# Optimization experiments

Hardware: AMD Instinct MI355X
Metric: run time of the kernel (lower is better)

The kernel has to match this reference:

```python
import jax, jax.numpy as jnp
import numpy as np
from jax import lax

EPS = 1e-8

def setup_inputs() -> dict:
    key = jax.random.key(0)
    k1, k2, k3, k4 = jax.random.split(key, 4)
    b, ic, oc, ks, sd, h, w = 16, 512, 512, 3, 512, 64, 64
    x = jax.random.normal(k1, (b, ic, h, w), dtype=jnp.float32)
    style = jax.random.normal(k2, (b, sd), dtype=jnp.float32)
    # kaiming_normal_(fan_in, linear): std = 1/sqrt(ic*ks*ks)
    weight = jax.random.normal(k3, (oc, ic, ks, ks), dtype=jnp.float32) / np.sqrt(ic * ks * ks)
    bias = jnp.zeros((oc,), dtype=jnp.float32)
    # nn.Linear default init ~ U(-1/sqrt(sd), 1/sqrt(sd)); normal approx is fine for a baseline
    mod_w = jax.random.normal(k4, (ic, sd), dtype=jnp.float32) / np.sqrt(sd)
    mod_b = jnp.ones((ic,), dtype=jnp.float32)  # bias initialized to 1.0 in the module
    return {"x": x, "style": style, "weight": weight, "bias": bias, "mod_w": mod_w, "mod_b": mod_b}

def reference(x, style, weight, bias, mod_w, mod_b):
    b, ic, h, w = x.shape
    oc, _, ks, _ = weight.shape
    # style modulation: [b, ic]
    s = style @ mod_w.T + mod_b
    # per-sample modulated weights: [b, oc, ic, k, k]
    wmod = weight[None] * s[:, None, :, None, None]
    # demodulation
    demod = lax.rsqrt(jnp.sum(wmod * wmod, axis=(2, 3, 4)) + EPS)  # [b, oc]
    wmod = wmod * demod[:, :, None, None, None]
    pad = ks // 2
    # grouped conv with groups=b == per-sample conv: vmap over batch
    def conv1(xi, wi):  # xi: [ic,h,w], wi: [oc,ic,k,k]
        return lax.conv_general_dilated(
            xi[None], wi, window_strides=(1, 1),
            padding=[(pad, pad), (pad, pad)],
            dimension_numbers=("NCHW", "OIHW", "NCHW"))[0]
    out = jax.vmap(conv1)(x, wmod)  # [b, oc, h, w]
    return out + bias[None, :, None, None]
```

## Files before the change

kernel.cpp:

```cpp
#include <hip/hip_runtime.h>
#include <hip/hip_bf16.h>


typedef __bf16 bf16x8 __attribute__((ext_vector_type(8)));
typedef float  f32x4  __attribute__((ext_vector_type(4)));

#define IC   512
#define OC   512
#define HW   4096
#define KTOT 4608

typedef __attribute__((address_space(3))) unsigned lds_u32;
typedef const __attribute__((address_space(1))) unsigned glb_u32;
#define GLL16(gsrc, ldst) \
    __builtin_amdgcn_global_load_lds((glb_u32*)(gsrc), (lds_u32*)(ldst), 16, 0, 0)
#define VMW(N) asm volatile("s_waitcnt vmcnt(" #N ")" ::: "memory")
#define BAR()  asm volatile("s_barrier" ::: "memory")

__global__ __launch_bounds__(256) void style_mod_kernel(
    const float* __restrict__ style, const float* __restrict__ mod_w,
    const float* __restrict__ mod_b, float* __restrict__ s_out)
{
    int pair = blockIdx.x * 4 + (threadIdx.x >> 6);
    int lane = threadIdx.x & 63;
    int b = pair >> 9;
    int i = pair & 511;
    const float4* sv = (const float4*)(style + b * 512);
    const float4* wv = (const float4*)(mod_w + i * 512);
    float4 a0 = sv[lane * 2], a1 = sv[lane * 2 + 1];
    float4 w0 = wv[lane * 2], w1 = wv[lane * 2 + 1];
    float sum = a0.x*w0.x + a0.y*w0.y + a0.z*w0.z + a0.w*w0.w
              + a1.x*w1.x + a1.y*w1.y + a1.z*w1.z + a1.w*w1.w;
    #pragma unroll
    for (int off = 32; off; off >>= 1) sum += __shfl_xor(sum, off);
    if (lane == 0) s_out[pair] = sum + mod_b[i];
}

__global__ __launch_bounds__(256) void wmod_kernel(
    const float* __restrict__ weight,
    const float* __restrict__ s_in,
    __hip_bfloat16* __restrict__ wmod)
{
    int b  = blockIdx.x >> 9;
    int oc = blockIdx.x & 511;
    __shared__ float s_sh[512];
    __shared__ float red[256];
    int t = threadIdx.x;
    s_sh[t]       = s_in[b * 512 + t];
    s_sh[t + 256] = s_in[b * 512 + t + 256];
    __syncthreads();
    const float* wrow = weight + (size_t)oc * KTOT;
    float partial = 0.f;
    for (int e = t; e < KTOT; e += 256) {
        float v = wrow[e] * s_sh[e / 9];
        partial += v * v;
    }
    red[t] = partial;
    __syncthreads();
    #pragma unroll
    for (int off = 128; off; off >>= 1) {
        if (t < off) red[t] += red[t + off];
        __syncthreads();
    }
    float demod = rsqrtf(red[0] + 1e-8f);
    __hip_bfloat16* dst = wmod + (size_t)blockIdx.x * KTOT;
    for (int ep = t; ep < KTOT; ep += 256) {
        int tap = ep >> 9, ic = ep & 511;
        dst[ep] = __float2bfloat16(wrow[ic * 9 + tap] * s_sh[ic] * demod);
    }
}

__global__ void zero_row_kernel(__hip_bfloat16* xT) {
    ((unsigned*)(xT + ((size_t)blockIdx.x * 4097 + 4096) * 512))[threadIdx.x] = 0u;
}

__global__ __launch_bounds__(256) void xpose_kernel(
    const float* __restrict__ x, __hip_bfloat16* __restrict__ xT)
{
    __shared__ __align__(16) float tile[64][68];
    int b = blockIdx.z, ic0 = blockIdx.y * 64, p0 = blockIdx.x * 64;
    int t = threadIdx.x;
    const float* xb = x + ((size_t)b * 512 + ic0) * 4096 + p0;
    int rr = t >> 4, cc = (t & 15) * 4;
    #pragma unroll
    for (int i = 0; i < 4; ++i) {
        float4 v = *(const float4*)(xb + (size_t)(rr + i * 16) * 4096 + cc);
        *(float4*)&tile[rr + i * 16][cc] = v;
    }
    __syncthreads();
    int pr = t >> 2, io = (t & 3) * 16;
    __hip_bfloat16 obuf[16];
    #pragma unroll
    for (int j = 0; j < 16; ++j) obuf[j] = __float2bfloat16(tile[io + j][pr]);
    __hip_bfloat16* dst = xT + ((size_t)b * 4097 + p0 + pr) * 512 + ic0 + io;
    *(uint4*)dst       = *(uint4*)&obuf[0];
    *(uint4*)(dst + 8) = *(uint4*)&obuf[8];
}

__global__ __launch_bounds__(512, 2) void conv_kernel(
    const __hip_bfloat16* __restrict__ xT,
    const __hip_bfloat16* __restrict__ wmod,
    const float* __restrict__ bias,
    float* __restrict__ out)
{
    __shared__ __align__(16) __hip_bfloat16 Ash[4][256 * 32];
    __shared__ __align__(16) __hip_bfloat16 Bsh[4][256 * 32];

    const int t    = threadIdx.x;
    const int lane = t & 63;
    const int wid  = t >> 6;
    const int wm   = wid >> 2;
    const int wn   = wid & 3;
    const int lr   = lane & 15;
    const int lq   = lane >> 4;

    int bid = blockIdx.x;
    int xcd = bid & 7, idx = bid >> 3;
    int oc1 = idx & 1;
    int nt  = (idx >> 1) & 15;
    int bb  = (idx >> 5) & 1;
    int b   = xcd * 2 + bb;
    int oc0 = oc1 * 256, n0 = nt * 256;

    const __hip_bfloat16* wb = wmod + (size_t)(b * 512 + oc0) * KTOT;
    const __hip_bfloat16* xb = xT + (size_t)b * 4097 * 512;

    const int qoff = (((t & 3) ^ ((t >> 3) & 3)) * 8);
    const int srow = t >> 2;
    const int p0g  = n0 + srow;
    const int y0p  = p0g >> 6, x0p = p0g & 63;

    const __hip_bfloat16* pA0 = wb + (size_t)srow * KTOT + qoff;
    const __hip_bfloat16* pA1 = pA0 + (size_t)128 * KTOT;

    const int swq = (lq ^ ((lr >> 1) & 3)) * 8;
    const int arb = (wm * 128 + lr) * 32 + swq;
    const int brb = (wn * 64  + lr) * 32 + swq;

    f32x4 acc[8][4] = {};

    auto bptrs = [&](int tap, const __hip_bfloat16*& P0, const __hip_bfloat16*& P1) {
        int dy = tap / 3 - 1, dx = tap % 3 - 1;
        int sy = y0p + dy, sx = x0p + dx;
        int pix0 = ((((unsigned)sy)  < 64u) & (((unsigned)sx) < 64u)) ? ((sy  << 6) + sx) : 4096;
        int sy1 = sy + 2;
        int pix1 = ((((unsigned)sy1) < 64u) & (((unsigned)sx) < 64u)) ? ((sy1 << 6) + sx) : 4096;
        P0 = xb + (size_t)pix0 * 512 + qoff;
        P1 = xb + (size_t)pix1 * 512 + qoff;
    };

#define STAGE(SB, PA_OFF, Q0, Q1, B_OFF) { \
    GLL16(pA0 + (PA_OFF), &Ash[SB][t * 8]); \
    GLL16(pA1 + (PA_OFF), &Ash[SB][(t + 512) * 8]); \
    GLL16((Q0) + (B_OFF), &Bsh[SB][t * 8]); \
    GLL16((Q1) + (B_OFF), &Bsh[SB][(t + 512) * 8]); }

#define COMPUTE(CB) { \
    bf16x8 af[8], bf[4]; \
    _Pragma("unroll") for (int mi = 0; mi < 8; ++mi) \
        af[mi] = *(const bf16x8*)(&Ash[CB][arb + mi * 512]); \
    _Pragma("unroll") for (int ni = 0; ni < 4; ++ni) \
        bf[ni] = *(const bf16x8*)(&Bsh[CB][brb + ni * 512]); \
    __builtin_amdgcn_s_setprio(1); \
    _Pragma("unroll") for (int mi = 0; mi < 8; ++mi) \
        _Pragma("unroll") for (int ni = 0; ni < 4; ++ni) \
            acc[mi][ni] = __builtin_amdgcn_mfma_f32_16x16x32_bf16( \
                af[mi], bf[ni], acc[mi][ni], 0, 0, 0); \
    __builtin_amdgcn_s_setprio(0); }

    const __hip_bfloat16 *pB0, *pB1, *nB0, *nB1;
    bptrs(0, pB0, pB1);

    STAGE(0, 0,  pB0, pB1, 0);
    STAGE(1, 32, pB0, pB1, 32);
    STAGE(2, 64, pB0, pB1, 64);
    VMW(8);
    BAR();

    for (int tap = 0; tap < 8; ++tap) {
        bptrs(tap + 1, nB0, nB1);
        #pragma unroll
        for (int ch = 0; ch < 16; ++ch) {
            if (ch < 13) { STAGE((ch + 3) & 3, (ch + 3) * 32, pB0, pB1, (ch + 3) * 32); }
            else         { STAGE((ch + 3) & 3, (ch + 3) * 32, nB0, nB1, (ch - 13) * 32); }
            COMPUTE(ch & 3);
            VMW(8);
            BAR();
        }
        pA0 += 512; pA1 += 512;
        pB0 = nB0; pB1 = nB1;
    }
    #pragma unroll
    for (int ch = 0; ch < 16; ++ch) {
        if (ch <= 12) { STAGE((ch + 3) & 3, (ch + 3) * 32, pB0, pB1, (ch + 3) * 32); }
        COMPUTE(ch & 3);
        if      (ch < 13)  { VMW(8); BAR(); }
        else if (ch == 13) { VMW(4); BAR(); }
        else if (ch == 14) { VMW(0); BAR(); }
    }
#undef STAGE
#undef COMPUTE

    #pragma unroll
    for (int mi = 0; mi < 8; ++mi) {
        int oc = oc0 + wm * 128 + mi * 16 + lq * 4;
        #pragma unroll
        for (int ni = 0; ni < 4; ++ni) {
            int n = n0 + wn * 64 + ni * 16 + lr;
            #pragma unroll
            for (int v = 0; v < 4; ++v) {
                float r = acc[mi][ni][v] + bias[oc + v];
                out[((size_t)(b * OC + oc + v)) * HW + n] = r;
            }
        }
    }
}

extern "C" void kernel_launch(void* const* d_in, const int* in_sizes, int n_in,
                              void* d_out, int out_size, void* d_ws, size_t ws_size,
                              hipStream_t stream) {
    const float* x      = (const float*)d_in[0];
    const float* style  = (const float*)d_in[1];
    const float* weight = (const float*)d_in[2];
    const float* bias   = (const float*)d_in[3];
    const float* mod_w  = (const float*)d_in[4];
    const float* mod_b  = (const float*)d_in[5];
    float* out = (float*)d_out;

    float* s_ws = (float*)d_ws;
    __hip_bfloat16* wmod = (__hip_bfloat16*)((char*)d_ws + 32768);
    __hip_bfloat16* xT   = (__hip_bfloat16*)((char*)d_ws + 32768 + (size_t)16 * 512 * KTOT * 2);

    style_mod_kernel<<<2048, 256, 0, stream>>>(style, mod_w, mod_b, s_ws);
    wmod_kernel<<<16 * 512, 256, 0, stream>>>(weight, s_ws, wmod);
    zero_row_kernel<<<16, 256, 0, stream>>>(xT);
    dim3 tgrid(64, 8, 16);
    xpose_kernel<<<tgrid, 256, 0, stream>>>(x, xT);
    conv_kernel<<<512, 512, 0, stream>>>(xT, wmod, bias, out);
}
```

Measured before the change: 379.4 us.

## Restructure conv mainloop into 64-wide double buffer and batch wmod per oc

The conv kernel moves from a 4-stage 32-wide K pipeline to a 2-buffer 64-wide K pipeline with a new XOR swizzle. Each 64-K step is split into eight quarter phases that interleave LDS fragment loads, global-to-LDS loads and MFMA groups, separated by barriers and explicit lgkm/vm waits. The wmod kernel now handles one output channel for all 16 samples, loading the weight row once and computing demod from per-ic squared sums times s squared, which avoids re-reading weights per sample. The cost is many more barriers per step and larger LDS use in wmod, which may lower occupancy.

```diff
diff --git a/kernel.cpp b/kernel.cpp
--- a/kernel.cpp
+++ b/kernel.cpp
@@ -14,8 +14,12 @@
 typedef const __attribute__((address_space(1))) unsigned glb_u32;
 #define GLL16(gsrc, ldst) \
     __builtin_amdgcn_global_load_lds((glb_u32*)(gsrc), (lds_u32*)(ldst), 16, 0, 0)
-#define VMW(N) asm volatile("s_waitcnt vmcnt(" #N ")" ::: "memory")
-#define BAR()  asm volatile("s_barrier" ::: "memory")
+#define BAR()   asm volatile("s_barrier" ::: "memory")
+#define LGKM0() asm volatile("s_waitcnt lgkmcnt(0)" ::: "memory")
+
+template<int N> __device__ __forceinline__ void vmw() {
+    asm volatile("s_waitcnt vmcnt(%0)" :: "n"(N) : "memory");
+}
 
 __global__ __launch_bounds__(256) void style_mod_kernel(
     const float* __restrict__ style, const float* __restrict__ mod_w,
@@ -41,32 +45,41 @@
     const float* __restrict__ s_in,
     __hip_bfloat16* __restrict__ wmod)
 {
-    int b  = blockIdx.x >> 9;
-    int oc = blockIdx.x & 511;
-    __shared__ float s_sh[512];
-    __shared__ float red[256];
+    int oc = blockIdx.x;
+    __shared__ float w_sh[4608];
+    __shared__ float s_sh[8192];
+    __shared__ float q_sh[512];
+    __shared__ float demod_sh[16];
     int t = threadIdx.x;
-    s_sh[t]       = s_in[b * 512 + t];
-    s_sh[t + 256] = s_in[b * 512 + t + 256];
+    const float* wrow = weight + (size_t)oc * KTOT;
+    for (int e = t; e < 4608; e += 256) w_sh[e] = wrow[e];
+    for (int e = t; e < 8192; e += 256) s_sh[e] = s_in[e];
     __syncthreads();
-    const float* wrow = weight + (size_t)oc * KTOT;
-    float partial = 0.f;
-    for (int e = t; e < KTOT; e += 256) {
-        float v = wrow[e] * s_sh[e / 9];
-        partial += v * v;
-    }
-    red[t] = partial;
+    for (int ic = t; ic < 512; ic += 256) {
+        float q = 0.f;
+        #pragma unroll
+        for (int tap = 0; tap < 9; ++tap) { float w = w_sh[ic * 9 + tap]; q += w * w; }
+        q_sh[ic] = q;
+    }
     __syncthreads();
-    #pragma unroll
-    for (int off = 128; off; off >>= 1) {
-        if (t < off) red[t] += red[t + off];
-        __syncthreads();
-    }
-    float demod = rsqrtf(red[0] + 1e-8f);
-    __hip_bfloat16* dst = wmod + (size_t)blockIdx.x * KTOT;
-    for (int ep = t; ep < KTOT; ep += 256) {
-        int tap = ep >> 9, ic = ep & 511;
-        dst[ep] = __float2bfloat16(wrow[ic * 9 + tap] * s_sh[ic] * demod);
+    int bb = t >> 4, li = t & 15;
+    float part = 0.f;
+    for (int ic = li; ic < 512; ic += 16) {
+        float sv = s_sh[bb * 512 + ic];
+        part += q_sh[ic] * sv * sv;
+    }
+    #pragma unroll
+    for (int off = 8; off; off >>= 1) part += __shfl_xor(part, off, 16);
+    if (li == 0) demod_sh[bb] = rsqrtf(part + 1e-8f);
+    __syncthreads();
+    for (int b2 = 0; b2 < 16; ++b2) {
+        float dm = demod_sh[b2];
+        const float* srow = s_sh + b2 * 512;
+        __hip_bfloat16* dst = wmod + ((size_t)b2 * 512 + oc) * KTOT;
+        for (int ep = t; ep < 4608; ep += 256) {
+            int tap = ep >> 9, ic = ep & 511;
+            dst[ep] = __float2bfloat16(w_sh[ic * 9 + tap] * srow[ic] * dm);
+        }
     }
 }
 
@@ -103,8 +116,12 @@
     const float* __restrict__ bias,
     float* __restrict__ out)
 {
-    __shared__ __align__(16) __hip_bfloat16 Ash[4][256 * 32];
-    __shared__ __align__(16) __hip_bfloat16 Bsh[4][256 * 32];
+    __shared__ __align__(16) __hip_bfloat16 Ash[2][256 * 64];
+    __shared__ __align__(16) __hip_bfloat16 Bsh[2][256 * 64];
+    __hip_bfloat16* const Ash0 = &Ash[0][0];
+    __hip_bfloat16* const Ash1 = &Ash[1][0];
+    __hip_bfloat16* const Bsh0 = &Bsh[0][0];
+    __hip_bfloat16* const Bsh1 = &Bsh[1][0];
 
     const int t    = threadIdx.x;
     const int lane = t & 63;
@@ -125,81 +142,127 @@
     const __hip_bfloat16* wb = wmod + (size_t)(b * 512 + oc0) * KTOT;
     const __hip_bfloat16* xb = xT + (size_t)b * 4097 * 512;
 
-    const int qoff = (((t & 3) ^ ((t >> 3) & 3)) * 8);
-    const int srow = t >> 2;
+    const int qoff = (((t & 7) ^ ((t >> 3) & 7)) * 8);
+    const int srow = t >> 3;
     const int p0g  = n0 + srow;
     const int y0p  = p0g >> 6, x0p = p0g & 63;
 
     const __hip_bfloat16* pA0 = wb + (size_t)srow * KTOT + qoff;
-    const __hip_bfloat16* pA1 = pA0 + (size_t)128 * KTOT;
-
-    const int swq = (lq ^ ((lr >> 1) & 3)) * 8;
-    const int arb = (wm * 128 + lr) * 32 + swq;
-    const int brb = (wn * 64  + lr) * 32 + swq;
+    const __hip_bfloat16* pA1 = pA0 + (size_t)64  * KTOT;
+    const __hip_bfloat16* pA2 = pA0 + (size_t)128 * KTOT;
+    const __hip_bfloat16* pA3 = pA0 + (size_t)192 * KTOT;
+
+    const int aoff0 = (wm * 128 + lr) * 64 + ((lq       ^ (lr & 7)) * 8);
+    const int aoff1 = (wm * 128 + lr) * 64 + (((4 + lq) ^ (lr & 7)) * 8);
+    const int boff0 = (wn * 64  + lr) * 64 + ((lq       ^ (lr & 7)) * 8);
+    const int boff1 = (wn * 64  + lr) * 64 + (((4 + lq) ^ (lr & 7)) * 8);
 
     f32x4 acc[8][4] = {};
-
-    auto bptrs = [&](int tap, const __hip_bfloat16*& P0, const __hip_bfloat16*& P1) {
+    bf16x8 a0[8], a1[8], b0[4], b1[4];
+
+    const __hip_bfloat16 *pB0_, *pB1_, *pB2_, *pB3_, *nB0, *nB1, *nB2, *nB3;
+    auto bptrs = [&](int tap, const __hip_bfloat16*& P0, const __hip_bfloat16*& P1,
+                     const __hip_bfloat16*& P2, const __hip_bfloat16*& P3) {
         int dy = tap / 3 - 1, dx = tap % 3 - 1;
-        int sy = y0p + dy, sx = x0p + dx;
-        int pix0 = ((((unsigned)sy)  < 64u) & (((unsigned)sx) < 64u)) ? ((sy  << 6) + sx) : 4096;
-        int sy1 = sy + 2;
-        int pix1 = ((((unsigned)sy1) < 64u) & (((unsigned)sx) < 64u)) ? ((sy1 << 6) + sx) : 4096;
-        P0 = xb + (size_t)pix0 * 512 + qoff;
-        P1 = xb + (size_t)pix1 * 512 + qoff;
+        int sx = x0p + dx;
+        bool okx = ((unsigned)sx < 64u);
+        int sy0 = y0p + dy;
+        int q0 = (okx & ((unsigned)(sy0    ) < 64u)) ? ((sy0    ) * 64 + sx) : 4096;
+        int q1 = (okx & ((unsigned)(sy0 + 1) < 64u)) ? ((sy0 + 1) * 64 + sx) : 4096;
+        int q2 = (okx & ((unsigned)(sy0 + 2) < 64u)) ? ((sy0 + 2) * 64 + sx) : 4096;
+        int q3 = (okx & ((unsigned)(sy0 + 3) < 64u)) ? ((sy0 + 3) * 64 + sx) : 4096;
+        P0 = xb + (size_t)q0 * 512 + qoff;
+        P1 = xb + (size_t)q1 * 512 + qoff;
+        P2 = xb + (size_t)q2 * 512 + qoff;
+        P3 = xb + (size_t)q3 * 512 + qoff;
     };
 
-#define STAGE(SB, PA_OFF, Q0, Q1, B_OFF) { \
-    GLL16(pA0 + (PA_OFF), &Ash[SB][t * 8]); \
-    GLL16(pA1 + (PA_OFF), &Ash[SB][(t + 512) * 8]); \
-    GLL16((Q0) + (B_OFF), &Bsh[SB][t * 8]); \
-    GLL16((Q1) + (B_OFF), &Bsh[SB][(t + 512) * 8]); }
-
-#define COMPUTE(CB) { \
-    bf16x8 af[8], bf[4]; \
-    _Pragma("unroll") for (int mi = 0; mi < 8; ++mi) \
-        af[mi] = *(const bf16x8*)(&Ash[CB][arb + mi * 512]); \
-    _Pragma("unroll") for (int ni = 0; ni < 4; ++ni) \
-        bf[ni] = *(const bf16x8*)(&Bsh[CB][brb + ni * 512]); \
+#define MF16(M0, AF, BF) { \
     __builtin_amdgcn_s_setprio(1); \
-    _Pragma("unroll") for (int mi = 0; mi < 8; ++mi) \
+    _Pragma("unroll") for (int mi = 0; mi < 4; ++mi) \
         _Pragma("unroll") for (int ni = 0; ni < 4; ++ni) \
-            acc[mi][ni] = __builtin_amdgcn_mfma_f32_16x16x32_bf16( \
-                af[mi], bf[ni], acc[mi][ni], 0, 0, 0); \
+            acc[(M0) + mi][ni] = __builtin_amdgcn_mfma_f32_16x16x32_bf16( \
+                AF[(M0) + mi], BF[ni], acc[(M0) + mi][ni], 0, 0, 0); \
     __builtin_amdgcn_s_setprio(0); }
 
-    const __hip_bfloat16 *pB0, *pB1, *nB0, *nB1;
-    bptrs(0, pB0, pB1);
-
-    STAGE(0, 0,  pB0, pB1, 0);
-    STAGE(1, 32, pB0, pB1, 32);
-    STAGE(2, 64, pB0, pB1, 64);
-    VMW(8);
+#define ITER_BODY(CT1, SCA, SCB, SP0, SP1, SP2, SP3, TAIL, VN4) { \
+     \
+    _Pragma("unroll") for (int mi = 0; mi < 8; ++mi) a0[mi] = *(const bf16x8*)&Ash0[aoff0 + mi * 1024]; \
+    _Pragma("unroll") for (int ni = 0; ni < 4; ++ni) b0[ni] = *(const bf16x8*)&Bsh0[boff0 + ni * 1024]; \
+    GLL16(pB0_ + (CT1), &Bsh1[t * 8]); GLL16(pB1_ + (CT1), &Bsh1[(t + 512) * 8]); \
+    BAR(); LGKM0(); \
+    MF16(0, a0, b0); \
+    BAR(); \
+     \
+    _Pragma("unroll") for (int mi = 0; mi < 8; ++mi) a1[mi] = *(const bf16x8*)&Ash0[aoff1 + mi * 1024]; \
+    GLL16(pB2_ + (CT1), &Bsh1[(t + 1024) * 8]); GLL16(pB3_ + (CT1), &Bsh1[(t + 1536) * 8]); \
+    BAR(); LGKM0(); \
+    MF16(4, a0, b0); \
+    BAR(); \
+     \
+    _Pragma("unroll") for (int ni = 0; ni < 4; ++ni) b1[ni] = *(const bf16x8*)&Bsh0[boff1 + ni * 1024]; \
+    if (!(TAIL)) { GLL16(pA0 + (SCA), &Ash0[t * 8]); GLL16(pA1 + (SCA), &Ash0[(t + 512) * 8]); } \
+    BAR(); LGKM0(); \
+    MF16(0, a1, b1); \
+    BAR(); \
+     \
+    if (!(TAIL)) { GLL16(pA2 + (SCA), &Ash0[(t + 1024) * 8]); GLL16(pA3 + (SCA), &Ash0[(t + 1536) * 8]); } \
+    BAR(); \
+    MF16(4, a1, b1); \
+    vmw<VN4>(); \
+    BAR(); \
+     \
+    _Pragma("unroll") for (int mi = 0; mi < 8; ++mi) a0[mi] = *(const bf16x8*)&Ash1[aoff0 + mi * 1024]; \
+    _Pragma("unroll") for (int ni = 0; ni < 4; ++ni) b0[ni] = *(const bf16x8*)&Bsh1[boff0 + ni * 1024]; \
+    if (!(TAIL)) { GLL16((SP0) + (SCB), &Bsh0[t * 8]); GLL16((SP1) + (SCB), &Bsh0[(t + 512) * 8]); } \
+    BAR(); LGKM0(); \
+    MF16(0, a0, b0); \
+    BAR(); \
+     \
+    _Pragma("unroll") for (int mi = 0; mi < 8; ++mi) a1[mi] = *(const bf16x8*)&Ash1[aoff1 + mi * 1024]; \
+    if (!(TAIL)) { GLL16((SP2) + (SCB), &Bsh0[(t + 1024) * 8]); GLL16((SP3) + (SCB), &Bsh0[(t + 1536) * 8]); } \
+    BAR(); LGKM0(); \
+    MF16(4, a0, b0); \
+    BAR(); \
+     \
+    _Pragma("unroll") for (int ni = 0; ni < 4; ++ni) b1[ni] = *(const bf16x8*)&Bsh1[boff1 + ni * 1024]; \
+    if (!(TAIL)) { GLL16(pA0 + (SCA) + 64, &Ash1[t * 8]); GLL16(pA1 + (SCA) + 64, &Ash1[(t + 512) * 8]); } \
+    BAR(); LGKM0(); \
+    MF16(0, a1, b1); \
+    BAR(); \
+     \
+    if (!(TAIL)) { GLL16(pA2 + (SCA) + 64, &Ash1[(t + 1024) * 8]); GLL16(pA3 + (SCA) + 64, &Ash1[(t + 1536) * 8]); } \
+    BAR(); \
+    MF16(4, a1, b1); \
+    if (!(TAIL)) { vmw<4>(); } \
+    BAR(); \
+}
+
+    bptrs(0, pB0_, pB1_, pB2_, pB3_);
+    GLL16(pA0, &Ash0[t * 8]);            GLL16(pA1, &Ash0[(t + 512) * 8]);
+    GLL16(pA2, &Ash0[(t + 1024) * 8]);   GLL16(pA3, &Ash0[(t + 1536) * 8]);
+    GLL16(pB0_, &Bsh0[t * 8]);           GLL16(pB1_, &Bsh0[(t + 512) * 8]);
+    GLL16(pB2_, &Bsh0[(t + 1024) * 8]);  GLL16(pB3_, &Bsh0[(t + 1536) * 8]);
+    GLL16(pA0 + 64, &Ash1[t * 8]);          GLL16(pA1 + 64, &Ash1[(t + 512) * 8]);
+    GLL16(pA2 + 64, &Ash1[(t + 1024) * 8]); GLL16(pA3 + 64, &Ash1[(t + 1536) * 8]);
+    vmw<4>();
     BAR();
 
-    for (int tap = 0; tap < 8; ++tap) {
-        bptrs(tap + 1, nB0, nB1);
-        #pragma unroll
-        for (int ch = 0; ch < 16; ++ch) {
-            if (ch < 13) { STAGE((ch + 3) & 3, (ch + 3) * 32, pB0, pB1, (ch + 3) * 32); }
-            else         { STAGE((ch + 3) & 3, (ch + 3) * 32, nB0, nB1, (ch - 13) * 32); }
-            COMPUTE(ch & 3);
-            VMW(8);
-            BAR();
+    for (int T = 0; T < 9; ++T) {
+        ITER_BODY( 64, 128, 128, pB0_, pB1_, pB2_, pB3_, false, 4);
+        ITER_BODY(192, 256, 256, pB0_, pB1_, pB2_, pB3_, false, 4);
+        ITER_BODY(320, 384, 384, pB0_, pB1_, pB2_, pB3_, false, 4);
+        if (T < 8) {
+            bptrs(T + 1, nB0, nB1, nB2, nB3);
+            ITER_BODY(448, 512, 0, nB0, nB1, nB2, nB3, false, 4);
+            pA0 += 512; pA1 += 512; pA2 += 512; pA3 += 512;
+            pB0_ = nB0; pB1_ = nB1; pB2_ = nB2; pB3_ = nB3;
+        } else {
+            ITER_BODY(448, 0, 0, pB0_, pB1_, pB2_, pB3_, true, 0);
         }
-        pA0 += 512; pA1 += 512;
-        pB0 = nB0; pB1 = nB1;
-    }
-    #pragma unroll
-    for (int ch = 0; ch < 16; ++ch) {
-        if (ch <= 12) { STAGE((ch + 3) & 3, (ch + 3) * 32, pB0, pB1, (ch + 3) * 32); }
-        COMPUTE(ch & 3);
-        if      (ch < 13)  { VMW(8); BAR(); }
-        else if (ch == 13) { VMW(4); BAR(); }
-        else if (ch == 14) { VMW(0); BAR(); }
-    }
-#undef STAGE
-#undef COMPUTE
+    }
+#undef ITER_BODY
+#undef MF16
 
     #pragma unroll
     for (int mi = 0; mi < 8; ++mi) {
@@ -232,7 +295,7 @@
     __hip_bfloat16* xT   = (__hip_bfloat16*)((char*)d_ws + 32768 + (size_t)16 * 512 * KTOT * 2);
 
     style_mod_kernel<<<2048, 256, 0, stream>>>(style, mod_w, mod_b, s_ws);
-    wmod_kernel<<<16 * 512, 256, 0, stream>>>(weight, s_ws, wmod);
+    wmod_kernel<<<512, 256, 0, stream>>>(weight, s_ws, wmod);
     zero_row_kernel<<<16, 256, 0, stream>>>(xT);
     dim3 tgrid(64, 8, 16);
     xpose_kernel<<<tgrid, 256, 0, stream>>>(x, xT);
```

Measured after the change: 869.2 us. 2.29x slower.
